# Performance work log

Hardware: AMD Instinct MI355X
Metric: run time of the kernel (lower is better)

## Reference

```python
import jax, jax.numpy as jnp
import numpy as np

B, N, L, D, H, GOUT = 256, 307, 12, 16, 8, 32


def pos_encoding():
    # positional_encoding(X, 16): P[1, L, D]
    pos = jnp.arange(L, dtype=jnp.float32)[:, None]
    div = jnp.power(10000.0, jnp.arange(0, D, 2, dtype=jnp.float32) / D)
    ang = pos / div  # [L, D/2]
    P = jnp.zeros((L, D), dtype=jnp.float32)
    P = P.at[:, 0::2].set(jnp.sin(ang)).at[:, 1::2].set(jnp.cos(ang))
    return P[None]  # [1, L, D]


def setup_inputs() -> dict:
    key = jax.random.key(0)
    ks = jax.random.split(key, 24)
    s = 0.02
    inp = {
        "flow_x": jax.random.normal(ks[0], (B, N, L), dtype=jnp.float32),
        "day_cyc": jax.random.randint(ks[1], (B, L), 0, 289),
        "week_cyc": jax.random.randint(ks[2], (B, L), 0, 8),
        "adj": (jax.random.uniform(ks[3], (N, N)) < 0.03).astype(jnp.float32),
        "day_emb": jax.random.normal(ks[4], (289, D), dtype=jnp.float32) * s,
        "week_emb": jax.random.normal(ks[5], (8, D), dtype=jnp.float32) * s,
        "Wq": jax.random.normal(ks[6], (D, D), dtype=jnp.float32) * s,
        "bq": jnp.zeros((D,), jnp.float32),
        "Wk": jax.random.normal(ks[7], (D, D), dtype=jnp.float32) * s,
        "bk": jnp.zeros((D,), jnp.float32),
        "Wv": jax.random.normal(ks[8], (D, D), dtype=jnp.float32) * s,
        "bv": jnp.zeros((D,), jnp.float32),
        "Wo": jax.random.normal(ks[9], (D, D), dtype=jnp.float32) * s,
        "bo": jnp.zeros((D,), jnp.float32),
        "Wg": jax.random.normal(ks[10], (1, GOUT), dtype=jnp.float32) * s,
        "Wt": jax.random.normal(ks[11], (D, GOUT), dtype=jnp.float32) * s,
        "bg": jnp.zeros((GOUT,), jnp.float32),
        "W1": jax.random.normal(ks[12], (N, GOUT, 8), dtype=jnp.float32) * s,
        "b1": jnp.zeros((N, 8), jnp.float32),
        "W2": jax.random.normal(ks[13], (N, 8, 1), dtype=jnp.float32) * s,
        "b2": jnp.zeros((N, 1), jnp.float32),
    }
    return inp


def dyn_graph(flow_x):
    # his_win[:, 0:12] = flow_x[0]; his_win[:, 11+b] = flow_x[b, :, -1] for b>=1
    his = jnp.concatenate([flow_x[0], flow_x[1:, :, -1].T], axis=1)  # [N, 11+B]
    sq = jnp.sum(his * his, axis=1)
    d2 = sq[:, None] + sq[None, :] - 2.0 * (his @ his.T)
    return jnp.sqrt(jnp.maximum(d2, 0.0))  # [N, N] euclidean distances


def reference(flow_x, day_cyc, week_cyc, adj, day_emb, week_emb,
              Wq, bq, Wk, bk, Wv, bv, Wo, bo, Wg, Wt, bg, W1, b1, W2, b2):
    hd = D // H  # head dim = 2
    fun_graph = dyn_graph(flow_x)                          # [N, N]
    pe = pos_encoding()                                    # [1, L, D]
    te = day_emb[day_cyc] + week_emb[week_cyc]             # [B, L, D]
    x_t = flow_x[..., None] + pe[:, None] + te[:, None]    # [B, N, L, D]

    # multi-head self-attention over time axis (8 heads, dim 16)
    def heads(x, W, b):
        return (x @ W + b).reshape(x.shape[0], x.shape[1], L, H, hd)
    q, k, v = heads(x_t, Wq, bq), heads(x_t, Wk, bk), heads(x_t, Wv, bv)
    logits = jnp.einsum('bnlhd,bnmhd->bnhlm', q, k) / jnp.sqrt(jnp.float32(hd))
    att = jnp.einsum('bnhlm,bnmhd->bnlhd', jax.nn.softmax(logits, axis=-1), v)
    att = att.reshape(flow_x.shape[0], N, L, D) @ Wo + bo
    x_tcn = x_t + att                                      # [B, N, L, D]

    # graph-temporal block: dynamic-graph message passing + static-graph mix
    A_dyn = jax.nn.softmax(-fun_graph, axis=-1)            # closer vertices weigh more
    A_st = adj / (jnp.sum(adj, axis=-1, keepdims=True) + 1.0)
    x_gcn = flow_x[..., None]                              # [B, N, L, 1]
    hid = jax.nn.relu(
        jnp.einsum('nm,bmlc->bnlc', A_dyn, x_gcn @ Wg)
        + jnp.einsum('nm,bmlc->bnlc', A_st, x_tcn @ Wt)
        + bg)                                              # [B, N, L, 32]

    # per-vertex 2-layer MLPs, batched over N (replaces the Python loop)
    h1 = jax.nn.relu(jnp.einsum('bnlc,nco->bnlo', hid, W1) + b1[None, :, None])
    out = jnp.einsum('bnlo,noz->bnlz', h1, W2) + b2[None, :, None]
    return out[..., 0]                                     # [B, N, 12]
```

## Files before the change

kernel.cpp:

```cpp
#include <hip/hip_runtime.h>
#include <hip/hip_bf16.h>
#include <math.h>

#define NB 256
#define NN 307
#define NBN 78592
#define LL 12
#define DDIM 16
#define HISW 268
#define HIS4 67
#define NBRCAP 64
#define AGRP 16
#define ADTS 308

#define OFF_XTCN 0u
#define OFF_G1   15089664u
#define OFF_ADT  16032768u
#define OFF_TEQ  16127456u
#define OFF_HIS  16176608u
#define OFF_TEK  16176608u
#define OFF_NW   16258896u
#define OFF_NIDX 16278544u
#define OFF_NCNT 16298192u
#define OFF_TEV  16298512u
#define OFF_TEO  16347664u

__device__ inline float4 mkf4(float a, float b, float c, float d) {
    float4 r; r.x = a; r.y = b; r.z = c; r.w = d; return r;
}

__global__ void his_kernel(const float* __restrict__ flow, float* __restrict__ his) {
    int e = blockIdx.x * 256 + threadIdx.x;
    if (e >= NN * HISW) return;
    int n = e / HISW, j = e - n * HISW;
    float v = 0.f;
    if (j < LL) v = flow[n * LL + j];
    else if (j < 267) v = flow[((j - 11) * NN + n) * LL + 11];
    his[e] = v;
}

__global__ __launch_bounds__(256) void te_kernel(
    const int* __restrict__ dayc, const int* __restrict__ weekc,
    const float* __restrict__ demb, const float* __restrict__ wemb,
    const float* __restrict__ Wq, const float* __restrict__ bq,
    const float* __restrict__ Wk, const float* __restrict__ bk,
    const float* __restrict__ Wv, const float* __restrict__ bv,
    const float* __restrict__ bo,
    float* __restrict__ TEQ, float* __restrict__ TEK,
    float* __restrict__ TEV, float* __restrict__ TEO) {
    __shared__ float sTE[16][16];
    int t = threadIdx.x, r = t >> 4, d = t & 15;
    int row = blockIdx.x * 16 + r;
    int b = row / LL, l = row - b * LL;
    int dc = dayc[b * LL + l], wc = weekc[b * LL + l];
    int i = d >> 1;
    float ang = (float)l * powf(10000.f, -0.125f * (float)i);
    float pe = (d & 1) ? cosf(ang) : sinf(ang);
    float te = demb[dc * DDIM + d] + wemb[wc * DDIM + d] + pe;
    sTE[r][d] = te;
    __syncthreads();
    float aq = bq[d], ak = bk[d], av = bv[d];
#pragma unroll
    for (int e = 0; e < 16; e++) {
        float x = sTE[r][e];
        aq += x * Wq[e * 16 + d];
        ak += x * Wk[e * 16 + d];
        av += x * Wv[e * 16 + d];
    }
    TEQ[row * 16 + d] = aq * 0.70710678118654752f;
    TEK[row * 16 + d] = ak;
    TEV[row * 16 + d] = av;
    TEO[row * 16 + d] = te + bo[d];
}

__global__ __launch_bounds__(256) void adyn_kernel(const float* __restrict__ his,
                                                   float* __restrict__ AdT) {
    __shared__ float4 sh[HIS4];
    __shared__ float red[256];
    int n = blockIdx.x, t = threadIdx.x;
    if (t < HIS4) sh[t] = reinterpret_cast<const float4*>(his)[n * HIS4 + t];
    __syncthreads();

    float e0 = 0.f, e1 = 0.f, lsum = 0.f;
    {
        const float4* row = reinterpret_cast<const float4*>(his) + t * HIS4;
        float4 acc = mkf4(0.f, 0.f, 0.f, 0.f);
        for (int j = 0; j < HIS4; j++) {
            float4 a = sh[j], b = row[j];
            float dx = a.x - b.x, dy = a.y - b.y, dz = a.z - b.z, dw = a.w - b.w;
            acc.x += dx * dx; acc.y += dy * dy; acc.z += dz * dz; acc.w += dw * dw;
        }
        float d2 = (acc.x + acc.y) + (acc.z + acc.w);
        e0 = __expf(-sqrtf(fmaxf(d2, 0.f)));
        lsum += e0;
    }
    int m1 = t + 256;
    if (m1 < NN) {
        const float4* row = reinterpret_cast<const float4*>(his) + m1 * HIS4;
        float4 acc = mkf4(0.f, 0.f, 0.f, 0.f);
        for (int j = 0; j < HIS4; j++) {
            float4 a = sh[j], b = row[j];
            float dx = a.x - b.x, dy = a.y - b.y, dz = a.z - b.z, dw = a.w - b.w;
            acc.x += dx * dx; acc.y += dy * dy; acc.z += dz * dz; acc.w += dw * dw;
        }
        float d2 = (acc.x + acc.y) + (acc.z + acc.w);
        e1 = __expf(-sqrtf(fmaxf(d2, 0.f)));
        lsum += e1;
    }
    red[t] = lsum;
    __syncthreads();
    for (int s = 128; s > 0; s >>= 1) {
        if (t < s) red[t] += red[t + s];
        __syncthreads();
    }
    float inv = 1.f / red[0];
    AdT[t * ADTS + n] = e0 * inv;
    if (m1 < NN) AdT[m1 * ADTS + n] = e1 * inv;
}

__global__ __launch_bounds__(64) void nbr_kernel(const float* __restrict__ adj,
                                                 int* __restrict__ ncnt,
                                                 int* __restrict__ nidx,
                                                 float* __restrict__ nw) {
    int n = blockIdx.x, t = threadIdx.x;
    float rs = 0.f;
    for (int m0 = 0; m0 < NN; m0 += 64) {
        int m = m0 + t;
        if (m < NN) rs += adj[n * NN + m];
    }
    for (int off = 32; off > 0; off >>= 1) rs += __shfl_xor(rs, off);
    float inv = 1.f / (rs + 1.f);
    int c = 0;
    for (int m0 = 0; m0 < NN; m0 += 64) {
        int m = m0 + t;
        float a = (m < NN) ? adj[n * NN + m] : 0.f;
        bool p = (a != 0.f);
        unsigned long long mask = __ballot(p);
        int pos = __popcll(mask & ((1ull << t) - 1ull));
        if (p && (c + pos) < NBRCAP) {
            nidx[n * NBRCAP + c + pos] = m;
            nw[n * NBRCAP + c + pos] = a * inv;
        }
        c += (int)__popcll(mask);
    }
    if (t == 0) ncnt[n] = c < NBRCAP ? c : NBRCAP;
}

__global__ __launch_bounds__(192) void attn_kernel(
    const float* __restrict__ flow,
    const float* __restrict__ TEQ, const float* __restrict__ TEK,
    const float* __restrict__ TEV, const float* __restrict__ TEO,
    const float* __restrict__ Wq, const float* __restrict__ Wk,
    const float* __restrict__ Wv, const float* __restrict__ Wo,
    unsigned short* __restrict__ xtcn) {
    __shared__ __align__(16) float sWo[256];
    __shared__ __align__(16) float sWs[48];
    __shared__ __align__(16) float sT[4][24][16];
    __shared__ __align__(16) float sA[AGRP][LL][20];

    const int t = threadIdx.x;
    const int bn0 = blockIdx.x * AGRP;
    const int b0 = bn0 / NN;
    const int rbase = b0 * LL;

    for (int id = t; id < 256; id += 192) sWo[id] = Wo[id];
    if (t < 48) {
        int mat = t >> 4, d = t & 15;
        const float* W = (mat == 0) ? Wq : (mat == 1) ? Wk : Wv;
        float s = 0.f;
#pragma unroll
        for (int e = 0; e < 16; e++) s += W[e * 16 + d];
        sWs[t] = (mat == 0) ? s * 0.70710678118654752f : s;
    }
#pragma unroll
    for (int p = 0; p < 2; p++) {
        int idx = t + p * 192;
        int tab = idx / 96, rr4 = idx - tab * 96;
        int rr = rr4 >> 2, j = rr4 & 3;
        int row = rbase + rr;
        if (row < NB * LL) {
            const float* src = (tab == 0) ? TEQ : (tab == 1) ? TEK : (tab == 2) ? TEV : TEO;
            reinterpret_cast<float4*>(&sT[tab][rr][0])[j] =
                reinterpret_cast<const float4*>(src + row * 16)[j];
        }
    }
    __syncthreads();

    if (t < AGRP * 8) {
        int g = t >> 3, h = t & 7;
        int bn = bn0 + g;
        int b = bn / NN;
        int lb = (b - b0) * LL;
        float f[12];
        {
            const float4* fr = reinterpret_cast<const float4*>(flow + bn * LL);
            float4 f0 = fr[0], f1 = fr[1], f2 = fr[2];
            f[0] = f0.x; f[1] = f0.y; f[2] = f0.z; f[3] = f0.w;
            f[4] = f1.x; f[5] = f1.y; f[6] = f1.z; f[7] = f1.w;
            f[8] = f2.x; f[9] = f2.y; f[10] = f2.z; f[11] = f2.w;
        }
        float wqx = sWs[2 * h], wqy = sWs[2 * h + 1];
        float wkx = sWs[16 + 2 * h], wky = sWs[16 + 2 * h + 1];
        float wvx = sWs[32 + 2 * h], wvy = sWs[32 + 2 * h + 1];
        float kx[12], ky[12], vx[12], vy[12];
#pragma unroll
        for (int m = 0; m < LL; m++) {
            float2 tk = *reinterpret_cast<const float2*>(&sT[1][lb + m][2 * h]);
            float2 tv = *reinterpret_cast<const float2*>(&sT[2][lb + m][2 * h]);
            kx[m] = tk.x + f[m] * wkx; ky[m] = tk.y + f[m] * wky;
            vx[m] = tv.x + f[m] * wvx; vy[m] = tv.y + f[m] * wvy;
        }
#pragma unroll
        for (int l = 0; l < LL; l++) {
            float2 tq = *reinterpret_cast<const float2*>(&sT[0][lb + l][2 * h]);
            float qx = tq.x + f[l] * wqx, qy = tq.y + f[l] * wqy;
            float s[12];
            float sum = 0.f;
#pragma unroll
            for (int m = 0; m < LL; m++) {
                s[m] = __expf(qx * kx[m] + qy * ky[m]);
                sum += s[m];
            }
            float a0 = 0.f, a1 = 0.f;
#pragma unroll
            for (int m = 0; m < LL; m++) { a0 += s[m] * vx[m]; a1 += s[m] * vy[m]; }
            float inv = 1.f / sum;
            float2 r; r.x = a0 * inv; r.y = a1 * inv;
            *reinterpret_cast<float2*>(&sA[g][l][2 * h]) = r;
        }
    }
    __syncthreads();

    {
        int g = t / LL, l = t - g * LL;
        int bn = bn0 + g;
        int b = bn / NN;
        int lb = (b - b0) * LL;
        float f = flow[bn * LL + l];
        float att[16];
        const float4* ar = reinterpret_cast<const float4*>(&sA[g][l][0]);
        float4 a0 = ar[0], a1 = ar[1], a2 = ar[2], a3 = ar[3];
        att[0] = a0.x; att[1] = a0.y; att[2] = a0.z; att[3] = a0.w;
        att[4] = a1.x; att[5] = a1.y; att[6] = a1.z; att[7] = a1.w;
        att[8] = a2.x; att[9] = a2.y; att[10] = a2.z; att[11] = a2.w;
        att[12] = a3.x; att[13] = a3.y; att[14] = a3.z; att[15] = a3.w;
        float o[16];
        const float4* to4 = reinterpret_cast<const float4*>(&sT[3][lb + l][0]);
#pragma unroll
        for (int j = 0; j < 4; j++) {
            float4 a = to4[j];
            o[4 * j] = a.x; o[4 * j + 1] = a.y; o[4 * j + 2] = a.z; o[4 * j + 3] = a.w;
        }
#pragma unroll
        for (int e = 0; e < 16; e++) {
            float ae = att[e];
            const float4* wo = reinterpret_cast<const float4*>(&sWo[e * 16]);
#pragma unroll
            for (int j = 0; j < 4; j++) {
                float4 w = wo[j];
                o[4 * j] += ae * w.x; o[4 * j + 1] += ae * w.y;
                o[4 * j + 2] += ae * w.z; o[4 * j + 3] += ae * w.w;
            }
        }
        unsigned pk[8];
#pragma unroll
        for (int j = 0; j < 8; j++) {
            unsigned u0 = __float_as_uint(o[2 * j] + f) + 0x8000u;
            unsigned u1 = __float_as_uint(o[2 * j + 1] + f) + 0x8000u;
            pk[j] = (u0 >> 16) | (u1 & 0xffff0000u);
        }
        uint4* dst = reinterpret_cast<uint4*>(xtcn + (size_t)bn * 192 + l * 16);
        uint4 d0; d0.x = pk[0]; d0.y = pk[1]; d0.z = pk[2]; d0.w = pk[3];
        uint4 d1; d1.x = pk[4]; d1.y = pk[5]; d1.z = pk[6]; d1.w = pk[7];
        dst[0] = d0; dst[1] = d1;
    }
}

__global__ __launch_bounds__(256) void g1_kernel(const float* __restrict__ flow,
                                                 const float* __restrict__ AdT,
                                                 float* __restrict__ G1) {
    int bp = blockIdx.x, nt = blockIdx.y, t = threadIdx.x;
    int lane = t & 63;
    int l0 = (t >> 6) * 3;
    int l0u = __builtin_amdgcn_readfirstlane(l0);
    int n = nt * 128 + 2 * lane;
    int b0 = 2 * bp;
    const float* fb0 = flow + (size_t)b0 * (NN * LL);
    const float* fb1 = fb0 + NN * LL;

    float a000 = 0.f, a001 = 0.f, a002 = 0.f;
    float a010 = 0.f, a011 = 0.f, a012 = 0.f;
    float a100 = 0.f, a101 = 0.f, a102 = 0.f;
    float a110 = 0.f, a111 = 0.f, a112 = 0.f;
#pragma unroll 4
    for (int m = 0; m < NN; m++) {
        float2 w = reinterpret_cast<const float2*>(AdT + (size_t)m * ADTS + nt * 128)[lane];
        const float* r0 = fb0 + m * LL + l0u;
        const float* r1 = fb1 + m * LL + l0u;
        float p0 = r0[0], p1 = r0[1], p2 = r0[2];
        float q0 = r1[0], q1 = r1[1], q2 = r1[2];
        a000 += w.x * p0; a001 += w.x * p1; a002 += w.x * p2;
        a010 += w.y * p0; a011 += w.y * p1; a012 += w.y * p2;
        a100 += w.x * q0; a101 += w.x * q1; a102 += w.x * q2;
        a110 += w.y * q0; a111 += w.y * q1; a112 += w.y * q2;
    }
    if (n < NN) {
        float* d0 = G1 + ((size_t)b0 * NN + n) * LL + l0;
        d0[0] = a000; d0[1] = a001; d0[2] = a002;
        float* d1 = G1 + ((size_t)(b0 + 1) * NN + n) * LL + l0;
        d1[0] = a100; d1[1] = a101; d1[2] = a102;
    }
    if (n + 1 < NN) {
        float* d0 = G1 + ((size_t)b0 * NN + n + 1) * LL + l0;
        d0[0] = a010; d0[1] = a011; d0[2] = a012;
        float* d1 = G1 + ((size_t)(b0 + 1) * NN + n + 1) * LL + l0;
        d1[0] = a110; d1[1] = a111; d1[2] = a112;
    }
}

__global__ __launch_bounds__(256) void final_kernel(
    const unsigned short* __restrict__ xtcn, const float* __restrict__ G1,
    const float* __restrict__ Wg, const float* __restrict__ Wt,
    const float* __restrict__ bg, const float* __restrict__ W1,
    const float* __restrict__ b1, const float* __restrict__ W2,
    const float* __restrict__ b2, const int* __restrict__ ncnt,
    const int* __restrict__ nidx, const float* __restrict__ nw,
    float* __restrict__ out) {
    __shared__ __align__(16) float sWt[512];
    __shared__ __align__(16) float sW1[256];
    __shared__ __align__(16) float sWg[32];
    __shared__ __align__(16) float sBg[32];
    __shared__ float sB1[8], sW2[8];
    __shared__ __align__(16) float sY[4][240];
    __shared__ __align__(16) float4 sHID[4][120];
    __shared__ float sH1[4][96];

    int t = threadIdx.x;
    int by = blockIdx.x;
    int n  = blockIdx.y;
    int w = t >> 6, t64 = t & 63;
    int b = by * 4 + w;

    sW1[t] = W1[n * 256 + t];
    sWt[t] = Wt[t];
    sWt[t + 256] = Wt[t + 256];
    if (t < 32) sWg[t] = Wg[t];
    else if (t < 64) sBg[t - 32] = bg[t - 32];
    else if (t < 72) sB1[t - 64] = b1[n * 8 + (t - 64)];
    else if (t < 80) sW2[t - 72] = W2[n * 8 + (t - 72)];
    float vb2 = b2[n];
    int cnt = ncnt[n];
    __syncthreads();

    if (t64 < 48) {
        float y0 = 0.f, y1 = 0.f, y2 = 0.f, y3 = 0.f;
        const unsigned short* base = xtcn + (size_t)b * NN * 192;
        int i = 0;
        for (; i + 3 < cnt; i += 4) {
            int m0 = nidx[n * NBRCAP + i],     m1 = nidx[n * NBRCAP + i + 1];
            int m2 = nidx[n * NBRCAP + i + 2], m3 = nidx[n * NBRCAP + i + 3];
            float w0 = nw[n * NBRCAP + i],     w1 = nw[n * NBRCAP + i + 1];
            float w2 = nw[n * NBRCAP + i + 2], w3 = nw[n * NBRCAP + i + 3];
            uint2 p0 = reinterpret_cast<const uint2*>(base + m0 * 192)[t64];
            uint2 p1 = reinterpret_cast<const uint2*>(base + m1 * 192)[t64];
            uint2 p2 = reinterpret_cast<const uint2*>(base + m2 * 192)[t64];
            uint2 p3 = reinterpret_cast<const uint2*>(base + m3 * 192)[t64];
            y0 += w0 * __uint_as_float(p0.x << 16) + w1 * __uint_as_float(p1.x << 16)
                + w2 * __uint_as_float(p2.x << 16) + w3 * __uint_as_float(p3.x << 16);
            y1 += w0 * __uint_as_float(p0.x & 0xffff0000u) + w1 * __uint_as_float(p1.x & 0xffff0000u)
                + w2 * __uint_as_float(p2.x & 0xffff0000u) + w3 * __uint_as_float(p3.x & 0xffff0000u);
            y2 += w0 * __uint_as_float(p0.y << 16) + w1 * __uint_as_float(p1.y << 16)
                + w2 * __uint_as_float(p2.y << 16) + w3 * __uint_as_float(p3.y << 16);
            y3 += w0 * __uint_as_float(p0.y & 0xffff0000u) + w1 * __uint_as_float(p1.y & 0xffff0000u)
                + w2 * __uint_as_float(p2.y & 0xffff0000u) + w3 * __uint_as_float(p3.y & 0xffff0000u);
        }
        for (; i < cnt; i++) {
            int ma = nidx[n * NBRCAP + i];
            float wa = nw[n * NBRCAP + i];
            uint2 pa = reinterpret_cast<const uint2*>(base + ma * 192)[t64];
            y0 += wa * __uint_as_float(pa.x << 16);
            y1 += wa * __uint_as_float(pa.x & 0xffff0000u);
            y2 += wa * __uint_as_float(pa.y << 16);
            y3 += wa * __uint_as_float(pa.y & 0xffff0000u);
        }
        int l = t64 >> 2, p = (t64 & 3);
        reinterpret_cast<float4*>(&sY[w][l * 20])[p] = mkf4(y0, y1, y2, y3);
    }
    __syncthreads();

#pragma unroll
    for (int p = 0; p < 2; p++) {
        int jb = t + p * 256;
        if (jb < 384) {
            int w2 = jb / 96, c = jb - w2 * 96;
            int b2i = by * 4 + w2;
            int l = c >> 3, j = c & 7;
            float g = G1[((size_t)b2i * NN + n) * LL + l];
            float4 wg = reinterpret_cast<const float4*>(sWg)[j];
            float4 acc = reinterpret_cast<const float4*>(sBg)[j];
            acc.x += g * wg.x; acc.y += g * wg.y; acc.z += g * wg.z; acc.w += g * wg.w;
            const float4* yr = reinterpret_cast<const float4*>(&sY[w2][l * 20]);
            float4 v0 = yr[0], v1 = yr[1], v2 = yr[2], v3 = yr[3];
            float ye[16] = {v0.x, v0.y, v0.z, v0.w, v1.x, v1.y, v1.z, v1.w,
                            v2.x, v2.y, v2.z, v2.w, v3.x, v3.y, v3.z, v3.w};
#pragma unroll
            for (int d = 0; d < 16; d++) {
                float4 wt = reinterpret_cast<const float4*>(sWt)[d * 8 + j];
                acc.x += ye[d] * wt.x; acc.y += ye[d] * wt.y;
                acc.z += ye[d] * wt.z; acc.w += ye[d] * wt.w;
            }
            acc.x = fmaxf(acc.x, 0.f); acc.y = fmaxf(acc.y, 0.f);
            acc.z = fmaxf(acc.z, 0.f); acc.w = fmaxf(acc.w, 0.f);
            sHID[w2][l * 10 + j] = acc;
        }
    }
    __syncthreads();

#pragma unroll
    for (int p = 0; p < 2; p++) {
        int jb = t + p * 256;
        if (jb < 384) {
            int w2 = jb / 96, o = jb - w2 * 96;
            int l = o >> 3, oo = o & 7;
            float acc = sB1[oo];
            float he[32];
#pragma unroll
            for (int k = 0; k < 8; k++) {
                float4 hv = sHID[w2][l * 10 + k];
                he[4 * k + 0] = hv.x; he[4 * k + 1] = hv.y;
                he[4 * k + 2] = hv.z; he[4 * k + 3] = hv.w;
            }
#pragma unroll
            for (int c = 0; c < 32; c++) acc += he[c] * sW1[c * 8 + oo];
            sH1[w2][o] = fmaxf(acc, 0.f);
        }
    }
    __syncthreads();

    if (t < 48) {
        int w2 = t / 12, l = t - w2 * 12;
        int b2i = by * 4 + w2;
        float acc = vb2;
#pragma unroll
        for (int o = 0; o < 8; o++) acc += sH1[w2][l * 8 + o] * sW2[o];
        out[((size_t)b2i * NN + n) * LL + l] = acc;
    }
}

extern "C" void kernel_launch(void* const* d_in, const int* in_sizes, int n_in,
                              void* d_out, int out_size, void* d_ws, size_t ws_size,
                              hipStream_t stream) {
    const float* flow = (const float*)d_in[0];
    const int* dayc   = (const int*)d_in[1];
    const int* weekc  = (const int*)d_in[2];
    const float* adj  = (const float*)d_in[3];
    const float* demb = (const float*)d_in[4];
    const float* wemb = (const float*)d_in[5];
    const float* Wq = (const float*)d_in[6];  const float* bq = (const float*)d_in[7];
    const float* Wk = (const float*)d_in[8];  const float* bk = (const float*)d_in[9];
    const float* Wv = (const float*)d_in[10]; const float* bv = (const float*)d_in[11];
    const float* Wo = (const float*)d_in[12]; const float* bo = (const float*)d_in[13];
    const float* Wg = (const float*)d_in[14]; const float* Wt = (const float*)d_in[15];
    const float* bg = (const float*)d_in[16];
    const float* W1 = (const float*)d_in[17]; const float* b1 = (const float*)d_in[18];
    const float* W2 = (const float*)d_in[19]; const float* b2 = (const float*)d_in[20];
    float* out = (float*)d_out;
    float* ws  = (float*)d_ws;

    unsigned short* xtcn = (unsigned short*)(ws + 0);
    float* G1   = ws + OFF_G1;
    float* AdT  = ws + OFF_ADT;
    float* TEQ  = ws + OFF_TEQ;
    float* TEK  = ws + OFF_TEK;
    float* TEV  = ws + OFF_TEV;
    float* TEO  = ws + OFF_TEO;
    float* his  = ws + OFF_HIS;
    float* nw   = ws + OFF_NW;
    int*   nidx = (int*)(ws + OFF_NIDX);
    int*   ncnt = (int*)(ws + OFF_NCNT);

    his_kernel<<<(NN * HISW + 255) / 256, 256, 0, stream>>>(flow, his);
    adyn_kernel<<<NN, 256, 0, stream>>>(his, AdT);
    te_kernel<<<(NB * LL) / 16, 256, 0, stream>>>(dayc, weekc, demb, wemb,
                                                  Wq, bq, Wk, bk, Wv, bv, bo,
                                                  TEQ, TEK, TEV, TEO);
    nbr_kernel<<<NN, 64, 0, stream>>>(adj, ncnt, nidx, nw);
    attn_kernel<<<NBN / AGRP, 192, 0, stream>>>(flow, TEQ, TEK, TEV, TEO,
                                                Wq, Wk, Wv, Wo, xtcn);
    g1_kernel<<<dim3(NB / 2, 3), 256, 0, stream>>>(flow, AdT, G1);
    final_kernel<<<dim3(64, NN), 256, 0, stream>>>(xtcn, G1, Wg, Wt, bg, W1, b1, W2, b2,
                                                   ncnt, nidx, nw, out);
}
```

Measured before the change: 271.9 us.

## Merge prep kernels and process eight batches per final_kernel block

The his, te and nbr kernels become one prep_kernel that dispatches on block index, which removes two launches. final_kernel now handles 8 batches per block instead of 4, launches half as many blocks, and stages neighbour indices, weights and G1 in shared memory. W1 is stored transposed so it can be read as float4. TEK is moved to a separate workspace offset so it no longer aliases his. The cost is more shared memory per block and fewer blocks, which could lower occupancy.

Result: slower. 282.0 us (+3.7%).

```diff
diff --git a/kernel.cpp b/kernel.cpp
--- a/kernel.cpp
+++ b/kernel.cpp
@@ -14,11 +14,11 @@
 #define ADTS 308
 
 #define OFF_XTCN 0u
+#define OFF_TEK  7544832u
 #define OFF_G1   15089664u
 #define OFF_ADT  16032768u
 #define OFF_TEQ  16127456u
 #define OFF_HIS  16176608u
-#define OFF_TEK  16176608u
 #define OFF_NW   16258896u
 #define OFF_NIDX 16278544u
 #define OFF_NCNT 16298192u
@@ -28,49 +28,81 @@
 __device__ inline float4 mkf4(float a, float b, float c, float d) {
     float4 r; r.x = a; r.y = b; r.z = c; r.w = d; return r;
 }
-
-__global__ void his_kernel(const float* __restrict__ flow, float* __restrict__ his) {
-    int e = blockIdx.x * 256 + threadIdx.x;
-    if (e >= NN * HISW) return;
-    int n = e / HISW, j = e - n * HISW;
-    float v = 0.f;
-    if (j < LL) v = flow[n * LL + j];
-    else if (j < 267) v = flow[((j - 11) * NN + n) * LL + 11];
-    his[e] = v;
-}
-
-__global__ __launch_bounds__(256) void te_kernel(
+__device__ inline float bf_lo(unsigned u) { return __uint_as_float(u << 16); }
+__device__ inline float bf_hi(unsigned u) { return __uint_as_float(u & 0xffff0000u); }
+
+__global__ __launch_bounds__(256) void prep_kernel(
+    const float* __restrict__ flow,
     const int* __restrict__ dayc, const int* __restrict__ weekc,
     const float* __restrict__ demb, const float* __restrict__ wemb,
     const float* __restrict__ Wq, const float* __restrict__ bq,
     const float* __restrict__ Wk, const float* __restrict__ bk,
     const float* __restrict__ Wv, const float* __restrict__ bv,
-    const float* __restrict__ bo,
+    const float* __restrict__ bo, const float* __restrict__ adj,
+    float* __restrict__ his,
     float* __restrict__ TEQ, float* __restrict__ TEK,
-    float* __restrict__ TEV, float* __restrict__ TEO) {
+    float* __restrict__ TEV, float* __restrict__ TEO,
+    int* __restrict__ ncnt, int* __restrict__ nidx, float* __restrict__ nw) {
     __shared__ float sTE[16][16];
-    int t = threadIdx.x, r = t >> 4, d = t & 15;
-    int row = blockIdx.x * 16 + r;
-    int b = row / LL, l = row - b * LL;
-    int dc = dayc[b * LL + l], wc = weekc[b * LL + l];
-    int i = d >> 1;
-    float ang = (float)l * powf(10000.f, -0.125f * (float)i);
-    float pe = (d & 1) ? cosf(ang) : sinf(ang);
-    float te = demb[dc * DDIM + d] + wemb[wc * DDIM + d] + pe;
-    sTE[r][d] = te;
-    __syncthreads();
-    float aq = bq[d], ak = bk[d], av = bv[d];
-#pragma unroll
-    for (int e = 0; e < 16; e++) {
-        float x = sTE[r][e];
-        aq += x * Wq[e * 16 + d];
-        ak += x * Wk[e * 16 + d];
-        av += x * Wv[e * 16 + d];
-    }
-    TEQ[row * 16 + d] = aq * 0.70710678118654752f;
-    TEK[row * 16 + d] = ak;
-    TEV[row * 16 + d] = av;
-    TEO[row * 16 + d] = te + bo[d];
+    int bx = blockIdx.x, t = threadIdx.x;
+    if (bx < 322) {
+        int e = bx * 256 + t;
+        if (e < NN * HISW) {
+            int n = e / HISW, j = e - n * HISW;
+            float v = 0.f;
+            if (j < LL) v = flow[n * LL + j];
+            else if (j < 267) v = flow[((j - 11) * NN + n) * LL + 11];
+            his[e] = v;
+        }
+    } else if (bx < 514) {
+        int r = t >> 4, d = t & 15;
+        int row = (bx - 322) * 16 + r;
+        int b = row / LL, l = row - b * LL;
+        int dc = dayc[b * LL + l], wc = weekc[b * LL + l];
+        int i = d >> 1;
+        float ang = (float)l * powf(10000.f, -0.125f * (float)i);
+        float pe = (d & 1) ? cosf(ang) : sinf(ang);
+        float te = demb[dc * DDIM + d] + wemb[wc * DDIM + d] + pe;
+        sTE[r][d] = te;
+        __syncthreads();
+        float aq = bq[d], ak = bk[d], av = bv[d];
+#pragma unroll
+        for (int e = 0; e < 16; e++) {
+            float x = sTE[r][e];
+            aq += x * Wq[e * 16 + d];
+            ak += x * Wk[e * 16 + d];
+            av += x * Wv[e * 16 + d];
+        }
+        TEQ[row * 16 + d] = aq * 0.70710678118654752f;
+        TEK[row * 16 + d] = ak;
+        TEV[row * 16 + d] = av;
+        TEO[row * 16 + d] = te + bo[d];
+    } else {
+        if (t < 64) {
+            int n = bx - 514;
+            float rs = 0.f;
+            for (int m0 = 0; m0 < NN; m0 += 64) {
+                int m = m0 + t;
+                if (m < NN) rs += adj[n * NN + m];
+            }
+            for (int off = 32; off > 0; off >>= 1) rs += __shfl_xor(rs, off);
+            float inv = 1.f / (rs + 1.f);
+            int c = 0;
+            for (int m0 = 0; m0 < NN; m0 += 64) {
+                int m = m0 + t;
+                float a = (m < NN) ? adj[n * NN + m] : 0.f;
+                bool p = (a != 0.f);
+                unsigned long long mask = __ballot(p);
+                int pos = __popcll(mask & ((1ull << t) - 1ull));
+                if (p && (c + pos) < NBRCAP) {
+                    nidx[n * NBRCAP + c + pos] = m;
+                    nw[n * NBRCAP + c + pos] = a * inv;
+                }
+                c += (int)__popcll(mask);
+            }
+            if (t == 0) ncnt[n] = c < NBRCAP ? c : NBRCAP;
+        }
+    }
 }
 
 __global__ __launch_bounds__(256) void adyn_kernel(const float* __restrict__ his,
@@ -116,34 +148,6 @@
     float inv = 1.f / red[0];
     AdT[t * ADTS + n] = e0 * inv;
     if (m1 < NN) AdT[m1 * ADTS + n] = e1 * inv;
-}
-
-__global__ __launch_bounds__(64) void nbr_kernel(const float* __restrict__ adj,
-                                                 int* __restrict__ ncnt,
-                                                 int* __restrict__ nidx,
-                                                 float* __restrict__ nw) {
-    int n = blockIdx.x, t = threadIdx.x;
-    float rs = 0.f;
-    for (int m0 = 0; m0 < NN; m0 += 64) {
-        int m = m0 + t;
-        if (m < NN) rs += adj[n * NN + m];
-    }
-    for (int off = 32; off > 0; off >>= 1) rs += __shfl_xor(rs, off);
-    float inv = 1.f / (rs + 1.f);
-    int c = 0;
-    for (int m0 = 0; m0 < NN; m0 += 64) {
-        int m = m0 + t;
-        float a = (m < NN) ? adj[n * NN + m] : 0.f;
-        bool p = (a != 0.f);
-        unsigned long long mask = __ballot(p);
-        int pos = __popcll(mask & ((1ull << t) - 1ull));
-        if (p && (c + pos) < NBRCAP) {
-            nidx[n * NBRCAP + c + pos] = m;
-            nw[n * NBRCAP + c + pos] = a * inv;
-        }
-        c += (int)__popcll(mask);
-    }
-    if (t == 0) ncnt[n] = c < NBRCAP ? c : NBRCAP;
 }
 
 __global__ __launch_bounds__(192) void attn_kernel(
@@ -327,123 +331,138 @@
     const int* __restrict__ nidx, const float* __restrict__ nw,
     float* __restrict__ out) {
     __shared__ __align__(16) float sWt[512];
-    __shared__ __align__(16) float sW1[256];
+    __shared__ __align__(16) float sW1T[288];
     __shared__ __align__(16) float sWg[32];
     __shared__ __align__(16) float sBg[32];
-    __shared__ float sB1[8], sW2[8];
-    __shared__ __align__(16) float sY[4][240];
-    __shared__ __align__(16) float4 sHID[4][120];
-    __shared__ float sH1[4][96];
+    __shared__ __align__(16) float sB1[8], sW2[8];
+    __shared__ __align__(16) float sG1[8][12];
+    __shared__ int sNid[64];
+    __shared__ float sNw[64];
+    __shared__ __align__(16) float sY[8][240];
+    __shared__ __align__(16) float4 sHID[8][120];
+    __shared__ float sH1[8][96];
 
     int t = threadIdx.x;
     int by = blockIdx.x;
     int n  = blockIdx.y;
     int w = t >> 6, t64 = t & 63;
-    int b = by * 4 + w;
-
-    sW1[t] = W1[n * 256 + t];
+
+    {
+        float v = W1[n * 256 + t];
+        sW1T[(t & 7) * 36 + (t >> 3)] = v;
+    }
     sWt[t] = Wt[t];
     sWt[t + 256] = Wt[t + 256];
     if (t < 32) sWg[t] = Wg[t];
     else if (t < 64) sBg[t - 32] = bg[t - 32];
     else if (t < 72) sB1[t - 64] = b1[n * 8 + (t - 64)];
     else if (t < 80) sW2[t - 72] = W2[n * 8 + (t - 72)];
+    else if (t < 144) sNid[t - 80] = nidx[n * NBRCAP + (t - 80)];
+    else if (t < 208) sNw[t - 144] = nw[n * NBRCAP + (t - 144)];
+    if (t < 96) {
+        int j = t / 12, l = t - j * 12;
+        sG1[j][l] = G1[((size_t)(by * 8 + j) * NN + n) * LL + l];
+    }
     float vb2 = b2[n];
     int cnt = ncnt[n];
     __syncthreads();
 
     if (t64 < 48) {
-        float y0 = 0.f, y1 = 0.f, y2 = 0.f, y3 = 0.f;
-        const unsigned short* base = xtcn + (size_t)b * NN * 192;
+        const unsigned short* baseA = xtcn + (size_t)(by * 8 + w) * (NN * 192);
+        const unsigned short* baseB = baseA + (size_t)4 * NN * 192;
+        float yA0 = 0.f, yA1 = 0.f, yA2 = 0.f, yA3 = 0.f;
+        float yB0 = 0.f, yB1 = 0.f, yB2 = 0.f, yB3 = 0.f;
         int i = 0;
-        for (; i + 3 < cnt; i += 4) {
-            int m0 = nidx[n * NBRCAP + i],     m1 = nidx[n * NBRCAP + i + 1];
-            int m2 = nidx[n * NBRCAP + i + 2], m3 = nidx[n * NBRCAP + i + 3];
-            float w0 = nw[n * NBRCAP + i],     w1 = nw[n * NBRCAP + i + 1];
-            float w2 = nw[n * NBRCAP + i + 2], w3 = nw[n * NBRCAP + i + 3];
-            uint2 p0 = reinterpret_cast<const uint2*>(base + m0 * 192)[t64];
-            uint2 p1 = reinterpret_cast<const uint2*>(base + m1 * 192)[t64];
-            uint2 p2 = reinterpret_cast<const uint2*>(base + m2 * 192)[t64];
-            uint2 p3 = reinterpret_cast<const uint2*>(base + m3 * 192)[t64];
-            y0 += w0 * __uint_as_float(p0.x << 16) + w1 * __uint_as_float(p1.x << 16)
-                + w2 * __uint_as_float(p2.x << 16) + w3 * __uint_as_float(p3.x << 16);
-            y1 += w0 * __uint_as_float(p0.x & 0xffff0000u) + w1 * __uint_as_float(p1.x & 0xffff0000u)
-                + w2 * __uint_as_float(p2.x & 0xffff0000u) + w3 * __uint_as_float(p3.x & 0xffff0000u);
-            y2 += w0 * __uint_as_float(p0.y << 16) + w1 * __uint_as_float(p1.y << 16)
-                + w2 * __uint_as_float(p2.y << 16) + w3 * __uint_as_float(p3.y << 16);
-            y3 += w0 * __uint_as_float(p0.y & 0xffff0000u) + w1 * __uint_as_float(p1.y & 0xffff0000u)
-                + w2 * __uint_as_float(p2.y & 0xffff0000u) + w3 * __uint_as_float(p3.y & 0xffff0000u);
-        }
-        for (; i < cnt; i++) {
-            int ma = nidx[n * NBRCAP + i];
-            float wa = nw[n * NBRCAP + i];
-            uint2 pa = reinterpret_cast<const uint2*>(base + ma * 192)[t64];
-            y0 += wa * __uint_as_float(pa.x << 16);
-            y1 += wa * __uint_as_float(pa.x & 0xffff0000u);
-            y2 += wa * __uint_as_float(pa.y << 16);
-            y3 += wa * __uint_as_float(pa.y & 0xffff0000u);
-        }
-        int l = t64 >> 2, p = (t64 & 3);
-        reinterpret_cast<float4*>(&sY[w][l * 20])[p] = mkf4(y0, y1, y2, y3);
-    }
-    __syncthreads();
-
-#pragma unroll
-    for (int p = 0; p < 2; p++) {
+        for (; i + 1 < cnt; i += 2) {
+            int m0 = sNid[i], m1 = sNid[i + 1];
+            float w0 = sNw[i], w1 = sNw[i + 1];
+            uint2 pA0 = reinterpret_cast<const uint2*>(baseA + m0 * 192)[t64];
+            uint2 pA1 = reinterpret_cast<const uint2*>(baseA + m1 * 192)[t64];
+            uint2 pB0 = reinterpret_cast<const uint2*>(baseB + m0 * 192)[t64];
+            uint2 pB1 = reinterpret_cast<const uint2*>(baseB + m1 * 192)[t64];
+            yA0 += w0 * bf_lo(pA0.x) + w1 * bf_lo(pA1.x);
+            yA1 += w0 * bf_hi(pA0.x) + w1 * bf_hi(pA1.x);
+            yA2 += w0 * bf_lo(pA0.y) + w1 * bf_lo(pA1.y);
+            yA3 += w0 * bf_hi(pA0.y) + w1 * bf_hi(pA1.y);
+            yB0 += w0 * bf_lo(pB0.x) + w1 * bf_lo(pB1.x);
+            yB1 += w0 * bf_hi(pB0.x) + w1 * bf_hi(pB1.x);
+            yB2 += w0 * bf_lo(pB0.y) + w1 * bf_lo(pB1.y);
+            yB3 += w0 * bf_hi(pB0.y) + w1 * bf_hi(pB1.y);
+        }
+        if (i < cnt) {
+            int m0 = sNid[i];
+            float w0 = sNw[i];
+            uint2 pA0 = reinterpret_cast<const uint2*>(baseA + m0 * 192)[t64];
+            uint2 pB0 = reinterpret_cast<const uint2*>(baseB + m0 * 192)[t64];
+            yA0 += w0 * bf_lo(pA0.x); yA1 += w0 * bf_hi(pA0.x);
+            yA2 += w0 * bf_lo(pA0.y); yA3 += w0 * bf_hi(pA0.y);
+            yB0 += w0 * bf_lo(pB0.x); yB1 += w0 * bf_hi(pB0.x);
+            yB2 += w0 * bf_lo(pB0.y); yB3 += w0 * bf_hi(pB0.y);
+        }
+        int l = t64 >> 2, p = t64 & 3;
+        reinterpret_cast<float4*>(&sY[w][l * 20])[p] = mkf4(yA0, yA1, yA2, yA3);
+        reinterpret_cast<float4*>(&sY[w + 4][l * 20])[p] = mkf4(yB0, yB1, yB2, yB3);
+    }
+    __syncthreads();
+
+#pragma unroll
+    for (int p = 0; p < 3; p++) {
         int jb = t + p * 256;
-        if (jb < 384) {
-            int w2 = jb / 96, c = jb - w2 * 96;
-            int b2i = by * 4 + w2;
-            int l = c >> 3, j = c & 7;
-            float g = G1[((size_t)b2i * NN + n) * LL + l];
-            float4 wg = reinterpret_cast<const float4*>(sWg)[j];
-            float4 acc = reinterpret_cast<const float4*>(sBg)[j];
-            acc.x += g * wg.x; acc.y += g * wg.y; acc.z += g * wg.z; acc.w += g * wg.w;
-            const float4* yr = reinterpret_cast<const float4*>(&sY[w2][l * 20]);
-            float4 v0 = yr[0], v1 = yr[1], v2 = yr[2], v3 = yr[3];
-            float ye[16] = {v0.x, v0.y, v0.z, v0.w, v1.x, v1.y, v1.z, v1.w,
-                            v2.x, v2.y, v2.z, v2.w, v3.x, v3.y, v3.z, v3.w};
-#pragma unroll
-            for (int d = 0; d < 16; d++) {
-                float4 wt = reinterpret_cast<const float4*>(sWt)[d * 8 + j];
-                acc.x += ye[d] * wt.x; acc.y += ye[d] * wt.y;
-                acc.z += ye[d] * wt.z; acc.w += ye[d] * wt.w;
-            }
-            acc.x = fmaxf(acc.x, 0.f); acc.y = fmaxf(acc.y, 0.f);
-            acc.z = fmaxf(acc.z, 0.f); acc.w = fmaxf(acc.w, 0.f);
-            sHID[w2][l * 10 + j] = acc;
-        }
-    }
-    __syncthreads();
-
-#pragma unroll
-    for (int p = 0; p < 2; p++) {
+        int j = jb / 96, c = jb - j * 96;
+        int l = c >> 3, ch = c & 7;
+        float g = sG1[j][l];
+        float4 wg = reinterpret_cast<const float4*>(sWg)[ch];
+        float4 acc = reinterpret_cast<const float4*>(sBg)[ch];
+        acc.x += g * wg.x; acc.y += g * wg.y; acc.z += g * wg.z; acc.w += g * wg.w;
+        const float4* yr = reinterpret_cast<const float4*>(&sY[j][l * 20]);
+        float4 v0 = yr[0], v1 = yr[1], v2 = yr[2], v3 = yr[3];
+        float ye[16] = {v0.x, v0.y, v0.z, v0.w, v1.x, v1.y, v1.z, v1.w,
+                        v2.x, v2.y, v2.z, v2.w, v3.x, v3.y, v3.z, v3.w};
+#pragma unroll
+        for (int d = 0; d < 16; d++) {
+            float4 wt = reinterpret_cast<const float4*>(sWt)[d * 8 + ch];
+            acc.x += ye[d] * wt.x; acc.y += ye[d] * wt.y;
+            acc.z += ye[d] * wt.z; acc.w += ye[d] * wt.w;
+        }
+        acc.x = fmaxf(acc.x, 0.f); acc.y = fmaxf(acc.y, 0.f);
+        acc.z = fmaxf(acc.z, 0.f); acc.w = fmaxf(acc.w, 0.f);
+        sHID[j][l * 10 + ch] = acc;
+    }
+    __syncthreads();
+
+#pragma unroll
+    for (int p = 0; p < 3; p++) {
         int jb = t + p * 256;
-        if (jb < 384) {
-            int w2 = jb / 96, o = jb - w2 * 96;
-            int l = o >> 3, oo = o & 7;
-            float acc = sB1[oo];
-            float he[32];
-#pragma unroll
-            for (int k = 0; k < 8; k++) {
-                float4 hv = sHID[w2][l * 10 + k];
-                he[4 * k + 0] = hv.x; he[4 * k + 1] = hv.y;
-                he[4 * k + 2] = hv.z; he[4 * k + 3] = hv.w;
-            }
-#pragma unroll
-            for (int c = 0; c < 32; c++) acc += he[c] * sW1[c * 8 + oo];
-            sH1[w2][o] = fmaxf(acc, 0.f);
-        }
-    }
-    __syncthreads();
-
-    if (t < 48) {
-        int w2 = t / 12, l = t - w2 * 12;
-        int b2i = by * 4 + w2;
-        float acc = vb2;
-#pragma unroll
-        for (int o = 0; o < 8; o++) acc += sH1[w2][l * 8 + o] * sW2[o];
-        out[((size_t)b2i * NN + n) * LL + l] = acc;
+        int j = jb / 96, o = jb - j * 96;
+        int l = o >> 3, oo = o & 7;
+        float acc = sB1[oo];
+        float he[32];
+#pragma unroll
+        for (int k = 0; k < 8; k++) {
+            float4 hv = sHID[j][l * 10 + k];
+            he[4 * k + 0] = hv.x; he[4 * k + 1] = hv.y;
+            he[4 * k + 2] = hv.z; he[4 * k + 3] = hv.w;
+        }
+        const float4* w1r = reinterpret_cast<const float4*>(&sW1T[oo * 36]);
+#pragma unroll
+        for (int k = 0; k < 8; k++) {
+            float4 wv = w1r[k];
+            acc += he[4 * k] * wv.x + he[4 * k + 1] * wv.y
+                 + he[4 * k + 2] * wv.z + he[4 * k + 3] * wv.w;
+        }
+        sH1[j][o] = fmaxf(acc, 0.f);
+    }
+    __syncthreads();
+
+    if (t < 96) {
+        int j = t / 12, l = t - j * 12;
+        const float4* h4 = reinterpret_cast<const float4*>(&sH1[j][l * 8]);
+        float4 ha = h4[0], hb = h4[1];
+        const float4* w4 = reinterpret_cast<const float4*>(sW2);
+        float4 wa = w4[0], wb = w4[1];
+        float acc = vb2 + ha.x * wa.x + ha.y * wa.y + ha.z * wa.z + ha.w * wa.w
+                        + hb.x * wb.x + hb.y * wb.y + hb.z * wb.z + hb.w * wb.w;
+        out[((size_t)(by * 8 + j) * NN + n) * LL + l] = acc;
     }
 }
 
@@ -468,10 +487,10 @@
     float* ws  = (float*)d_ws;
 
     unsigned short* xtcn = (unsigned short*)(ws + 0);
+    float* TEK  = ws + OFF_TEK;
     float* G1   = ws + OFF_G1;
     float* AdT  = ws + OFF_ADT;
     float* TEQ  = ws + OFF_TEQ;
-    float* TEK  = ws + OFF_TEK;
     float* TEV  = ws + OFF_TEV;
     float* TEO  = ws + OFF_TEO;
     float* his  = ws + OFF_HIS;
@@ -479,15 +498,13 @@
     int*   nidx = (int*)(ws + OFF_NIDX);
     int*   ncnt = (int*)(ws + OFF_NCNT);
 
-    his_kernel<<<(NN * HISW + 255) / 256, 256, 0, stream>>>(flow, his);
+    prep_kernel<<<821, 256, 0, stream>>>(flow, dayc, weekc, demb, wemb,
+                                         Wq, bq, Wk, bk, Wv, bv, bo, adj,
+                                         his, TEQ, TEK, TEV, TEO, ncnt, nidx, nw);
     adyn_kernel<<<NN, 256, 0, stream>>>(his, AdT);
-    te_kernel<<<(NB * LL) / 16, 256, 0, stream>>>(dayc, weekc, demb, wemb,
-                                                  Wq, bq, Wk, bk, Wv, bv, bo,
-                                                  TEQ, TEK, TEV, TEO);
-    nbr_kernel<<<NN, 64, 0, stream>>>(adj, ncnt, nidx, nw);
     attn_kernel<<<NBN / AGRP, 192, 0, stream>>>(flow, TEQ, TEK, TEV, TEO,
                                                 Wq, Wk, Wv, Wo, xtcn);
     g1_kernel<<<dim3(NB / 2, 3), 256, 0, stream>>>(flow, AdT, G1);
-    final_kernel<<<dim3(64, NN), 256, 0, stream>>>(xtcn, G1, Wg, Wt, bg, W1, b1, W2, b2,
+    final_kernel<<<dim3(32, NN), 256, 0, stream>>>(xtcn, G1, Wg, Wt, bg, W1, b1, W2, b2,
                                                    ncnt, nidx, nw, out);
 }
```
